# Optimization experiments

Measured on AMD Instinct MI355X. Metric: run time of the kernel, lower is better.

Reference implementation:

```python
import jax, jax.numpy as jnp
import numpy as np
import math

B, S, D, H = 2, 2048, 768, 12
DK = D // H


def setup_inputs() -> dict:
    key = jax.random.key(0)
    ks = jax.random.split(key, 8)
    scale = 1.0 / math.sqrt(D)  # xavier-ish scale for weights
    inp = {
        "query": jax.random.normal(ks[0], (B, S, D), jnp.float32),
        "key": jax.random.normal(ks[1], (B, S, D), jnp.float32),
        "value": jax.random.normal(ks[2], (B, S, D), jnp.float32),
        # causal mask: True = masked (matches torch masked_fill_ semantics)
        "mask": jnp.broadcast_to(jnp.triu(jnp.ones((S, S), bool), k=1), (B, S, S)),
        "wq": jax.random.normal(ks[3], (D, D), jnp.float32) * scale,
        "wk": jax.random.normal(ks[4], (D, D), jnp.float32) * scale,
        "wv": jax.random.normal(ks[5], (D, D), jnp.float32) * scale,
        "wo": jax.random.normal(ks[6], (D, D), jnp.float32) * scale,
        "bo": jnp.zeros((D,), jnp.float32),
    }
    return inp


def reference(query, key, value, mask, wq, wk, wv, wo, bo):
    # nn.Linear stores weight [out, in]; y = x @ W^T
    def split_heads(x):  # [B,S,D] -> [B,H,S,DK]
        return x.reshape(B, S, H, DK).transpose(0, 2, 1, 3)

    q = split_heads(jnp.einsum('bsd,ed->bse', query, wq))
    k = split_heads(jnp.einsum('bsd,ed->bse', key, wk))
    v = split_heads(jnp.einsum('bsd,ed->bse', value, wv))

    scores = jnp.einsum('bhqd,bhkd->bhqk', q, k) / math.sqrt(DK)
    scores = jnp.where(mask[:, None, :, :], -jnp.inf, scores)
    attn = jax.nn.softmax(scores, axis=-1)  # dropout is identity in eval / p=0

    attended = jnp.einsum('bhqk,bhkd->bhqd', attn, v)
    attended = attended.transpose(0, 2, 1, 3).reshape(B, S, D)
    return jnp.einsum('bsd,ed->bse', attended, wo) + bo
```

## Files before the change

kernel.cpp:

```cpp
#include <hip/hip_runtime.h>

namespace {
constexpr int Sc = 2048, Dc = 768, Hc = 12, Mc = 4096;

using fragb = __attribute__((ext_vector_type(8))) short;
using f32x4 = __attribute__((ext_vector_type(4))) float;

#define MFMA16(A, B, C) __builtin_amdgcn_mfma_f32_16x16x32_bf16(A, B, C, 0, 0, 0)

__device__ __forceinline__ unsigned short bf16hi(float f) {
  unsigned int u = __float_as_uint(f);
  return (unsigned short)((u + 0x7fffu + ((u >> 16) & 1u)) >> 16);
}
__device__ __forceinline__ float fbf(unsigned short h) {
  return __uint_as_float((unsigned int)h << 16);
}
__device__ __forceinline__ unsigned int packsplit(float f) {
  unsigned short h = bf16hi(f);
  unsigned short l = bf16hi(f - fbf(h));
  return ((unsigned int)h << 16) | (unsigned int)l;
}
__device__ __forceinline__ void split8(const float* x, fragb& hv, fragb& lv) {
  union { fragb v; short s[8]; } h, l;
#pragma unroll
  for (int i = 0; i < 8; ++i) {
    unsigned short hh = bf16hi(x[i]);
    h.s[i] = (short)hh;
    l.s[i] = (short)bf16hi(x[i] - fbf(hh));
  }
  hv = h.v; lv = l.v;
}
__device__ __forceinline__ void unpack8(const unsigned int* u, fragb& hv, fragb& lv) {
  union { fragb v; short s[8]; } h, l;
#pragma unroll
  for (int i = 0; i < 8; ++i) {
    h.s[i] = (short)(u[i] >> 16);
    l.s[i] = (short)(u[i] & 0xffffu);
  }
  hv = h.v; lv = l.v;
}

template <int AMODE, int OMODE>
__global__ __launch_bounds__(256, 3) void proj_kernel(
    const void* __restrict__ Asrc, const float* __restrict__ W,
    const float* __restrict__ bias, void* __restrict__ Out)
{
  const int tid = threadIdx.x;
  const int lane = tid & 63, w = tid >> 6;
  const int g = lane >> 4, l15 = lane & 15;
  const int m0 = blockIdx.x * 64, n0 = blockIdx.y * 64;

  __shared__ __align__(16) short Ah[64][40], Al[64][40];
  __shared__ __align__(16) short Bh[64][40], Bl[64][40];

  f32x4 acc[4] = {};

  const int srow = tid >> 2;
  const int scol = (tid & 3) * 8;

  for (int k0 = 0; k0 < Dc; k0 += 32) {
    fragb ah_s, al_s, bh_s, bl_s;
    if (AMODE == 0) {
      const float* ap = (const float*)Asrc + (size_t)(m0 + srow) * Dc + k0 + scol;
      float4 v0 = *(const float4*)(ap);
      float4 v1 = *(const float4*)(ap + 4);
      float xa[8] = {v0.x, v0.y, v0.z, v0.w, v1.x, v1.y, v1.z, v1.w};
      split8(xa, ah_s, al_s);
    } else {
      const unsigned int* ap = (const unsigned int*)Asrc + (size_t)(m0 + srow) * Dc + k0 + scol;
      uint4 v0 = *(const uint4*)(ap);
      uint4 v1 = *(const uint4*)(ap + 4);
      unsigned int ua[8] = {v0.x, v0.y, v0.z, v0.w, v1.x, v1.y, v1.z, v1.w};
      unpack8(ua, ah_s, al_s);
    }
    {
      const float* wp = W + (size_t)(n0 + srow) * Dc + k0 + scol;
      float4 v0 = *(const float4*)(wp);
      float4 v1 = *(const float4*)(wp + 4);
      float xw[8] = {v0.x, v0.y, v0.z, v0.w, v1.x, v1.y, v1.z, v1.w};
      split8(xw, bh_s, bl_s);
    }
    __syncthreads();
    *(fragb*)&Ah[srow][scol] = ah_s;
    *(fragb*)&Al[srow][scol] = al_s;
    *(fragb*)&Bh[srow][scol] = bh_s;
    *(fragb*)&Bl[srow][scol] = bl_s;
    __syncthreads();

    const fragb aH = *(const fragb*)&Ah[16 * w + l15][8 * g];
    const fragb aL = *(const fragb*)&Al[16 * w + l15][8 * g];
#pragma unroll
    for (int nb = 0; nb < 4; ++nb) {
      const fragb bH = *(const fragb*)&Bh[nb * 16 + l15][8 * g];
      const fragb bL = *(const fragb*)&Bl[nb * 16 + l15][8 * g];
      acc[nb] = MFMA16(aH, bH, acc[nb]);
      acc[nb] = MFMA16(aH, bL, acc[nb]);
      acc[nb] = MFMA16(aL, bH, acc[nb]);
    }
  }

  const int mrow = m0 + 16 * w + 4 * g;
  if (OMODE == 2) {
#pragma unroll
    for (int nb = 0; nb < 4; ++nb) {
      const int n = n0 + nb * 16 + l15;
      const float bv = bias[n];
#pragma unroll
      for (int r = 0; r < 4; ++r)
        ((float*)Out)[(size_t)(mrow + r) * Dc + n] = acc[nb][r] + bv;
    }
  } else {
#pragma unroll
    for (int nb = 0; nb < 4; ++nb) {
      const int n = n0 + nb * 16 + l15;
      const int hh = n >> 6, dk = n & 63;
#pragma unroll
      for (int r = 0; r < 4; ++r) {
        const int m = mrow + r;
        const int bb = m >> 11, s = m & (Sc - 1);
        const size_t idx = (OMODE == 0)
            ? (((size_t)bb * Hc + hh) * Sc + s) * 64 + dk
            : (((size_t)bb * Hc + hh) * 64 + dk) * Sc + s;
        ((unsigned int*)Out)[idx] = packsplit(acc[nb][r]);
      }
    }
  }
}

__global__ __launch_bounds__(256, 3) void attn_kernel(
    const unsigned int* __restrict__ Qp, const unsigned int* __restrict__ Kp,
    const unsigned int* __restrict__ Vtg, unsigned int* __restrict__ att2)
{
  const int tid = threadIdx.x;
  const int lane = tid & 63, w = tid >> 6;
  const int g = lane >> 4, l15 = lane & 15;
  const int t = blockIdx.x;
  const int bh = blockIdx.y;
  const int b = bh / Hc, h = bh % Hc;

  const int qtile = (w < 2) ? t : (63 - t);
  const int qbase = qtile * 32 + (w & 1) * 16;
  const int ktmax = (qbase + 15) >> 6;
  const int NKT = ((Sc - 1 - 32 * t) >> 6) + 1;

  __shared__ __align__(16) short Ks_h[64][72], Ks_l[64][72];
  __shared__ __align__(16) short Vt_h[64][72], Vt_l[64][72];
  __shared__ __align__(16) short Ps[64][72];

  fragb qh[2], ql[2];
  {
    const unsigned int* qrow = Qp + ((size_t)bh * Sc + qbase + l15) * 64;
#pragma unroll
    for (int c = 0; c < 2; ++c) {
      uint4 v0 = *(const uint4*)(qrow + c * 32 + g * 8);
      uint4 v1 = *(const uint4*)(qrow + c * 32 + g * 8 + 4);
      unsigned int u[8] = {v0.x, v0.y, v0.z, v0.w, v1.x, v1.y, v1.z, v1.w};
      unpack8(u, qh[c], ql[c]);
    }
  }

  f32x4 oacc[4] = {};
  float m_run[4] = {-1e30f, -1e30f, -1e30f, -1e30f};
  float l_run[4] = {0.f, 0.f, 0.f, 0.f};

  const int srow = tid >> 2;
  const int scol = (tid & 3) * 16;

  for (int kt = 0; kt < NKT; ++kt) {
    const int k0 = kt * 64;
    uint4 ka[4], va[4];
    {
      const unsigned int* kp = Kp + ((size_t)bh * Sc + k0 + srow) * 64 + scol;
      const unsigned int* vp = Vtg + ((size_t)bh * 64 + srow) * Sc + k0 + scol;
#pragma unroll
      for (int u = 0; u < 4; ++u) {
        ka[u] = *(const uint4*)(kp + 4 * u);
        va[u] = *(const uint4*)(vp + 4 * u);
      }
    }
    __syncthreads();
    {
      fragb h0, l0, h1, l1;
      unsigned int u[8];
      u[0]=ka[0].x; u[1]=ka[0].y; u[2]=ka[0].z; u[3]=ka[0].w;
      u[4]=ka[1].x; u[5]=ka[1].y; u[6]=ka[1].z; u[7]=ka[1].w;
      unpack8(u, h0, l0);
      u[0]=ka[2].x; u[1]=ka[2].y; u[2]=ka[2].z; u[3]=ka[2].w;
      u[4]=ka[3].x; u[5]=ka[3].y; u[6]=ka[3].z; u[7]=ka[3].w;
      unpack8(u, h1, l1);
      *(fragb*)&Ks_h[srow][scol]     = h0;
      *(fragb*)&Ks_h[srow][scol + 8] = h1;
      *(fragb*)&Ks_l[srow][scol]     = l0;
      *(fragb*)&Ks_l[srow][scol + 8] = l1;
      u[0]=va[0].x; u[1]=va[0].y; u[2]=va[0].z; u[3]=va[0].w;
      u[4]=va[1].x; u[5]=va[1].y; u[6]=va[1].z; u[7]=va[1].w;
      unpack8(u, h0, l0);
      u[0]=va[2].x; u[1]=va[2].y; u[2]=va[2].z; u[3]=va[2].w;
      u[4]=va[3].x; u[5]=va[3].y; u[6]=va[3].z; u[7]=va[3].w;
      unpack8(u, h1, l1);
      *(fragb*)&Vt_h[srow][scol]     = h0;
      *(fragb*)&Vt_h[srow][scol + 8] = h1;
      *(fragb*)&Vt_l[srow][scol]     = l0;
      *(fragb*)&Vt_l[srow][scol + 8] = l1;
    }
    __syncthreads();

    if (kt <= ktmax) {
      f32x4 sacc[4] = {};
#pragma unroll
      for (int c = 0; c < 2; ++c) {
#pragma unroll
        for (int kb = 0; kb < 4; ++kb) {
          const fragb kH = *(const fragb*)&Ks_h[kb * 16 + l15][c * 32 + g * 8];
          const fragb kL = *(const fragb*)&Ks_l[kb * 16 + l15][c * 32 + g * 8];
          sacc[kb] = MFMA16(qh[c], kH, sacc[kb]);
          sacc[kb] = MFMA16(qh[c], kL, sacc[kb]);
          sacc[kb] = MFMA16(ql[c], kH, sacc[kb]);
        }
      }
      float p[4][4], mx[4];
#pragma unroll
      for (int r = 0; r < 4; ++r) {
        const int qrow = qbase + 4 * g + r;
#pragma unroll
        for (int kb = 0; kb < 4; ++kb) {
          const int kc = k0 + kb * 16 + l15;
          const float x = sacc[kb][r] * 0.125f;
          p[kb][r] = (kc > qrow) ? -1e30f : x;
        }
        mx[r] = fmaxf(fmaxf(p[0][r], p[1][r]), fmaxf(p[2][r], p[3][r]));
      }
#pragma unroll
      for (int off = 8; off > 0; off >>= 1)
#pragma unroll
        for (int r = 0; r < 4; ++r)
          mx[r] = fmaxf(mx[r], __shfl_xor(mx[r], off));
#pragma unroll
      for (int r = 0; r < 4; ++r) {
        const float mnew = fmaxf(m_run[r], mx[r]);
        const float alpha = __expf(m_run[r] - mnew);
        m_run[r] = mnew;
        float rs = 0.f;
#pragma unroll
        for (int kb = 0; kb < 4; ++kb) { p[kb][r] = __expf(p[kb][r] - mnew); rs += p[kb][r]; }
#pragma unroll
        for (int off = 8; off > 0; off >>= 1) rs += __shfl_xor(rs, off);
        l_run[r] = l_run[r] * alpha + rs;
#pragma unroll
        for (int db = 0; db < 4; ++db) oacc[db][r] *= alpha;
      }
      const int strip = 16 * w;
#pragma unroll
      for (int kb = 0; kb < 4; ++kb)
#pragma unroll
        for (int r = 0; r < 4; ++r)
          Ps[strip + 4 * g + r][kb * 16 + l15] = (short)bf16hi(p[kb][r]);
#pragma unroll
      for (int c = 0; c < 2; ++c) {
        const fragb pf = *(const fragb*)&Ps[strip + l15][c * 32 + g * 8];
#pragma unroll
        for (int db = 0; db < 4; ++db) {
          const fragb vH = *(const fragb*)&Vt_h[db * 16 + l15][c * 32 + g * 8];
          const fragb vL = *(const fragb*)&Vt_l[db * 16 + l15][c * 32 + g * 8];
          oacc[db] = MFMA16(pf, vH, oacc[db]);
          oacc[db] = MFMA16(pf, vL, oacc[db]);
        }
      }
    }
  }

#pragma unroll
  for (int r = 0; r < 4; ++r) {
    const float rl = 1.0f / l_run[r];
    const int s = qbase + 4 * g + r;
    unsigned int* orow = att2 + ((size_t)b * Sc + s) * Dc + h * 64 + l15;
#pragma unroll
    for (int db = 0; db < 4; ++db)
      orow[db * 16] = packsplit(oacc[db][r] * rl);
  }
}

}

extern "C" void kernel_launch(void* const* d_in, const int* in_sizes, int n_in,
                              void* d_out, int out_size, void* d_ws, size_t ws_size,
                              hipStream_t stream) {
  const float* q  = (const float*)d_in[0];
  const float* k  = (const float*)d_in[1];
  const float* v  = (const float*)d_in[2];
  const float* wq = (const float*)d_in[4];
  const float* wk = (const float*)d_in[5];
  const float* wv = (const float*)d_in[6];
  const float* wo = (const float*)d_in[7];
  const float* bo = (const float*)d_in[8];

  unsigned int* ws   = (unsigned int*)d_ws;
  const size_t NQ = (size_t)Mc * Dc;
  unsigned int* Qp   = ws;
  unsigned int* Kp   = ws + NQ;
  unsigned int* Vtg  = ws + 2 * NQ;
  unsigned int* att2 = ws + 3 * NQ;

  const dim3 blk(256);
  const dim3 gproj(Mc / 64, Dc / 64);
  const dim3 gattn(32, 2 * Hc);

  proj_kernel<0, 0><<<gproj, blk, 0, stream>>>(q, wq, nullptr, Qp);
  proj_kernel<0, 0><<<gproj, blk, 0, stream>>>(k, wk, nullptr, Kp);
  proj_kernel<0, 1><<<gproj, blk, 0, stream>>>(v, wv, nullptr, Vtg);
  attn_kernel<<<gattn, blk, 0, stream>>>(Qp, Kp, Vtg, att2);
  proj_kernel<1, 2><<<gproj, blk, 0, stream>>>(att2, wo, bo, d_out);
}
```

Before: 336.0 us.

## Store hi/lo bf16 planes separately and enlarge projection tile to 128 rows

Intermediate Q/K/V/attention tensors are now stored as two separate bf16 planes (hi and lo) instead of packed 32-bit words. This lets the attention and output-projection kernels copy tiles straight into shared memory without unpacking. The split now truncates instead of rounding to nearest. Projection blocks grow to 128x64 with B fragments reused across two M sub-tiles, and launch bounds move to 4 waves per SIMD. The cost is more scattered 2-byte stores in the projection epilogue and a small change in numerics from the truncating split.

```diff
diff --git a/kernel.cpp b/kernel.cpp
--- a/kernel.cpp
+++ b/kernel.cpp
@@ -8,128 +8,132 @@
 
 #define MFMA16(A, B, C) __builtin_amdgcn_mfma_f32_16x16x32_bf16(A, B, C, 0, 0, 0)
 
-__device__ __forceinline__ unsigned short bf16hi(float f) {
+__device__ __forceinline__ unsigned short bf16rne(float f) {
   unsigned int u = __float_as_uint(f);
   return (unsigned short)((u + 0x7fffu + ((u >> 16) & 1u)) >> 16);
 }
-__device__ __forceinline__ float fbf(unsigned short h) {
-  return __uint_as_float((unsigned int)h << 16);
-}
-__device__ __forceinline__ unsigned int packsplit(float f) {
-  unsigned short h = bf16hi(f);
-  unsigned short l = bf16hi(f - fbf(h));
-  return ((unsigned int)h << 16) | (unsigned int)l;
-}
-__device__ __forceinline__ void split8(const float* x, fragb& hv, fragb& lv) {
-  union { fragb v; short s[8]; } h, l;
-#pragma unroll
-  for (int i = 0; i < 8; ++i) {
-    unsigned short hh = bf16hi(x[i]);
-    h.s[i] = (short)hh;
-    l.s[i] = (short)bf16hi(x[i] - fbf(hh));
-  }
-  hv = h.v; lv = l.v;
-}
-__device__ __forceinline__ void unpack8(const unsigned int* u, fragb& hv, fragb& lv) {
-  union { fragb v; short s[8]; } h, l;
-#pragma unroll
-  for (int i = 0; i < 8; ++i) {
-    h.s[i] = (short)(u[i] >> 16);
-    l.s[i] = (short)(u[i] & 0xffffu);
-  }
-  hv = h.v; lv = l.v;
+__device__ __forceinline__ void splitt(float f, unsigned short& h, unsigned short& l) {
+  const unsigned int u = __float_as_uint(f);
+  h = (unsigned short)(u >> 16);
+  const float r = f - __uint_as_float(u & 0xffff0000u);
+  l = (unsigned short)(__float_as_uint(r) >> 16);
 }
 
 template <int AMODE, int OMODE>
-__global__ __launch_bounds__(256, 3) void proj_kernel(
-    const void* __restrict__ Asrc, const float* __restrict__ W,
-    const float* __restrict__ bias, void* __restrict__ Out)
+__global__ __launch_bounds__(256, 4) void proj_kernel(
+    const void* __restrict__ Asrc_h, const void* __restrict__ Asrc_l,
+    const float* __restrict__ W, const float* __restrict__ bias,
+    unsigned short* __restrict__ Oh, unsigned short* __restrict__ Ol,
+    float* __restrict__ Ofp)
 {
   const int tid = threadIdx.x;
   const int lane = tid & 63, w = tid >> 6;
   const int g = lane >> 4, l15 = lane & 15;
-  const int m0 = blockIdx.x * 64, n0 = blockIdx.y * 64;
-
-  __shared__ __align__(16) short Ah[64][40], Al[64][40];
-  __shared__ __align__(16) short Bh[64][40], Bl[64][40];
-
-  f32x4 acc[4] = {};
-
-  const int srow = tid >> 2;
-  const int scol = (tid & 3) * 8;
+  const int m0 = blockIdx.x * 128, n0 = blockIdx.y * 64;
+
+  __shared__ __align__(16) unsigned short Ah[128][40], Al[128][40];
+  __shared__ __align__(16) unsigned short Bh[64][40],  Bl[64][40];
+
+  f32x4 acc[2][4] = {};
+
+  const int arow = tid >> 1;
+  const int acol = (tid & 1) * 16;
+  const int brow = tid >> 2;
+  const int bcol = (tid & 3) * 8;
 
   for (int k0 = 0; k0 < Dc; k0 += 32) {
-    fragb ah_s, al_s, bh_s, bl_s;
+    unsigned short ah[16], al[16], bh[8], bl[8];
     if (AMODE == 0) {
-      const float* ap = (const float*)Asrc + (size_t)(m0 + srow) * Dc + k0 + scol;
-      float4 v0 = *(const float4*)(ap);
-      float4 v1 = *(const float4*)(ap + 4);
-      float xa[8] = {v0.x, v0.y, v0.z, v0.w, v1.x, v1.y, v1.z, v1.w};
-      split8(xa, ah_s, al_s);
+      const float* ap = (const float*)Asrc_h + (size_t)(m0 + arow) * Dc + k0 + acol;
+#pragma unroll
+      for (int i = 0; i < 16; i += 4) {
+        const float4 v = *(const float4*)(ap + i);
+        splitt(v.x, ah[i+0], al[i+0]); splitt(v.y, ah[i+1], al[i+1]);
+        splitt(v.z, ah[i+2], al[i+2]); splitt(v.w, ah[i+3], al[i+3]);
+      }
     } else {
-      const unsigned int* ap = (const unsigned int*)Asrc + (size_t)(m0 + srow) * Dc + k0 + scol;
-      uint4 v0 = *(const uint4*)(ap);
-      uint4 v1 = *(const uint4*)(ap + 4);
-      unsigned int ua[8] = {v0.x, v0.y, v0.z, v0.w, v1.x, v1.y, v1.z, v1.w};
-      unpack8(ua, ah_s, al_s);
+      const unsigned short* aph = (const unsigned short*)Asrc_h + (size_t)(m0 + arow) * Dc + k0 + acol;
+      const unsigned short* apl = (const unsigned short*)Asrc_l + (size_t)(m0 + arow) * Dc + k0 + acol;
+      *(uint4*)&ah[0] = *(const uint4*)(aph);
+      *(uint4*)&ah[8] = *(const uint4*)(aph + 8);
+      *(uint4*)&al[0] = *(const uint4*)(apl);
+      *(uint4*)&al[8] = *(const uint4*)(apl + 8);
     }
     {
-      const float* wp = W + (size_t)(n0 + srow) * Dc + k0 + scol;
-      float4 v0 = *(const float4*)(wp);
-      float4 v1 = *(const float4*)(wp + 4);
-      float xw[8] = {v0.x, v0.y, v0.z, v0.w, v1.x, v1.y, v1.z, v1.w};
-      split8(xw, bh_s, bl_s);
+      const float* wp = W + (size_t)(n0 + brow) * Dc + k0 + bcol;
+#pragma unroll
+      for (int i = 0; i < 8; i += 4) {
+        const float4 v = *(const float4*)(wp + i);
+        splitt(v.x, bh[i+0], bl[i+0]); splitt(v.y, bh[i+1], bl[i+1]);
+        splitt(v.z, bh[i+2], bl[i+2]); splitt(v.w, bh[i+3], bl[i+3]);
+      }
     }
     __syncthreads();
-    *(fragb*)&Ah[srow][scol] = ah_s;
-    *(fragb*)&Al[srow][scol] = al_s;
-    *(fragb*)&Bh[srow][scol] = bh_s;
-    *(fragb*)&Bl[srow][scol] = bl_s;
+    *(uint4*)&Ah[arow][acol]     = *(uint4*)&ah[0];
+    *(uint4*)&Ah[arow][acol + 8] = *(uint4*)&ah[8];
+    *(uint4*)&Al[arow][acol]     = *(uint4*)&al[0];
+    *(uint4*)&Al[arow][acol + 8] = *(uint4*)&al[8];
+    *(uint4*)&Bh[brow][bcol]     = *(uint4*)&bh[0];
+    *(uint4*)&Bl[brow][bcol]     = *(uint4*)&bl[0];
     __syncthreads();
 
-    const fragb aH = *(const fragb*)&Ah[16 * w + l15][8 * g];
-    const fragb aL = *(const fragb*)&Al[16 * w + l15][8 * g];
+    fragb bHf[4], bLf[4];
 #pragma unroll
     for (int nb = 0; nb < 4; ++nb) {
-      const fragb bH = *(const fragb*)&Bh[nb * 16 + l15][8 * g];
-      const fragb bL = *(const fragb*)&Bl[nb * 16 + l15][8 * g];
-      acc[nb] = MFMA16(aH, bH, acc[nb]);
-      acc[nb] = MFMA16(aH, bL, acc[nb]);
-      acc[nb] = MFMA16(aL, bH, acc[nb]);
-    }
-  }
-
-  const int mrow = m0 + 16 * w + 4 * g;
-  if (OMODE == 2) {
-#pragma unroll
-    for (int nb = 0; nb < 4; ++nb) {
-      const int n = n0 + nb * 16 + l15;
-      const float bv = bias[n];
-#pragma unroll
-      for (int r = 0; r < 4; ++r)
-        ((float*)Out)[(size_t)(mrow + r) * Dc + n] = acc[nb][r] + bv;
-    }
-  } else {
-#pragma unroll
-    for (int nb = 0; nb < 4; ++nb) {
-      const int n = n0 + nb * 16 + l15;
-      const int hh = n >> 6, dk = n & 63;
-#pragma unroll
-      for (int r = 0; r < 4; ++r) {
-        const int m = mrow + r;
-        const int bb = m >> 11, s = m & (Sc - 1);
-        const size_t idx = (OMODE == 0)
-            ? (((size_t)bb * Hc + hh) * Sc + s) * 64 + dk
-            : (((size_t)bb * Hc + hh) * 64 + dk) * Sc + s;
-        ((unsigned int*)Out)[idx] = packsplit(acc[nb][r]);
+      bHf[nb] = *(const fragb*)&Bh[nb * 16 + l15][8 * g];
+      bLf[nb] = *(const fragb*)&Bl[nb * 16 + l15][8 * g];
+    }
+#pragma unroll
+    for (int s = 0; s < 2; ++s) {
+      const fragb aH = *(const fragb*)&Ah[32 * w + 16 * s + l15][8 * g];
+      const fragb aL = *(const fragb*)&Al[32 * w + 16 * s + l15][8 * g];
+#pragma unroll
+      for (int nb = 0; nb < 4; ++nb) {
+        acc[s][nb] = MFMA16(aH, bHf[nb], acc[s][nb]);
+        acc[s][nb] = MFMA16(aH, bLf[nb], acc[s][nb]);
+        acc[s][nb] = MFMA16(aL, bHf[nb], acc[s][nb]);
+      }
+    }
+  }
+
+#pragma unroll
+  for (int s = 0; s < 2; ++s) {
+    const int mrow = m0 + 32 * w + 16 * s + 4 * g;
+    if (OMODE == 2) {
+#pragma unroll
+      for (int nb = 0; nb < 4; ++nb) {
+        const int n = n0 + nb * 16 + l15;
+        const float bv = bias[n];
+#pragma unroll
+        for (int r = 0; r < 4; ++r)
+          Ofp[(size_t)(mrow + r) * Dc + n] = acc[s][nb][r] + bv;
+      }
+    } else {
+#pragma unroll
+      for (int nb = 0; nb < 4; ++nb) {
+        const int n = n0 + nb * 16 + l15;
+        const int hh = n >> 6, dk = n & 63;
+#pragma unroll
+        for (int r = 0; r < 4; ++r) {
+          const int m = mrow + r;
+          const int bb = m >> 11, ss = m & (Sc - 1);
+          const size_t idx = (OMODE == 0)
+              ? (((size_t)bb * Hc + hh) * Sc + ss) * 64 + dk
+              : (((size_t)bb * Hc + hh) * 64 + dk) * Sc + ss;
+          unsigned short h, l;
+          splitt(acc[s][nb][r], h, l);
+          Oh[idx] = h; Ol[idx] = l;
+        }
       }
     }
   }
 }
 
 __global__ __launch_bounds__(256, 3) void attn_kernel(
-    const unsigned int* __restrict__ Qp, const unsigned int* __restrict__ Kp,
-    const unsigned int* __restrict__ Vtg, unsigned int* __restrict__ att2)
+    const unsigned short* __restrict__ Qh, const unsigned short* __restrict__ Ql,
+    const unsigned short* __restrict__ Kh, const unsigned short* __restrict__ Kl,
+    const unsigned short* __restrict__ Vth, const unsigned short* __restrict__ Vtl,
+    unsigned short* __restrict__ Aoh, unsigned short* __restrict__ Aol)
 {
   const int tid = threadIdx.x;
   const int lane = tid & 63, w = tid >> 6;
@@ -143,19 +147,18 @@
   const int ktmax = (qbase + 15) >> 6;
   const int NKT = ((Sc - 1 - 32 * t) >> 6) + 1;
 
-  __shared__ __align__(16) short Ks_h[64][72], Ks_l[64][72];
-  __shared__ __align__(16) short Vt_h[64][72], Vt_l[64][72];
-  __shared__ __align__(16) short Ps[64][72];
-
-  fragb qh[2], ql[2];
+  __shared__ __align__(16) unsigned short Ks_h[64][72], Ks_l[64][72];
+  __shared__ __align__(16) unsigned short Vt_h[64][72], Vt_l[64][72];
+  __shared__ __align__(16) unsigned short Ps[64][72];
+
+  fragb qfh[2], qfl[2];
   {
-    const unsigned int* qrow = Qp + ((size_t)bh * Sc + qbase + l15) * 64;
+    const unsigned short* qrh = Qh + ((size_t)bh * Sc + qbase + l15) * 64;
+    const unsigned short* qrl = Ql + ((size_t)bh * Sc + qbase + l15) * 64;
 #pragma unroll
     for (int c = 0; c < 2; ++c) {
-      uint4 v0 = *(const uint4*)(qrow + c * 32 + g * 8);
-      uint4 v1 = *(const uint4*)(qrow + c * 32 + g * 8 + 4);
-      unsigned int u[8] = {v0.x, v0.y, v0.z, v0.w, v1.x, v1.y, v1.z, v1.w};
-      unpack8(u, qh[c], ql[c]);
+      qfh[c] = *(const fragb*)(qrh + c * 32 + g * 8);
+      qfl[c] = *(const fragb*)(qrl + c * 32 + g * 8);
     }
   }
 
@@ -168,41 +171,26 @@
 
   for (int kt = 0; kt < NKT; ++kt) {
     const int k0 = kt * 64;
-    uint4 ka[4], va[4];
+    uint4 st[8];
     {
-      const unsigned int* kp = Kp + ((size_t)bh * Sc + k0 + srow) * 64 + scol;
-      const unsigned int* vp = Vtg + ((size_t)bh * 64 + srow) * Sc + k0 + scol;
-#pragma unroll
-      for (int u = 0; u < 4; ++u) {
-        ka[u] = *(const uint4*)(kp + 4 * u);
-        va[u] = *(const uint4*)(vp + 4 * u);
-      }
+      const unsigned short* kph = Kh  + ((size_t)bh * Sc + k0 + srow) * 64 + scol;
+      const unsigned short* kpl = Kl  + ((size_t)bh * Sc + k0 + srow) * 64 + scol;
+      const unsigned short* vph = Vth + ((size_t)bh * 64 + srow) * Sc + k0 + scol;
+      const unsigned short* vpl = Vtl + ((size_t)bh * 64 + srow) * Sc + k0 + scol;
+      st[0] = *(const uint4*)(kph);  st[1] = *(const uint4*)(kph + 8);
+      st[2] = *(const uint4*)(kpl);  st[3] = *(const uint4*)(kpl + 8);
+      st[4] = *(const uint4*)(vph);  st[5] = *(const uint4*)(vph + 8);
+      st[6] = *(const uint4*)(vpl);  st[7] = *(const uint4*)(vpl + 8);
     }
     __syncthreads();
-    {
-      fragb h0, l0, h1, l1;
-      unsigned int u[8];
-      u[0]=ka[0].x; u[1]=ka[0].y; u[2]=ka[0].z; u[3]=ka[0].w;
-      u[4]=ka[1].x; u[5]=ka[1].y; u[6]=ka[1].z; u[7]=ka[1].w;
-      unpack8(u, h0, l0);
-      u[0]=ka[2].x; u[1]=ka[2].y; u[2]=ka[2].z; u[3]=ka[2].w;
-      u[4]=ka[3].x; u[5]=ka[3].y; u[6]=ka[3].z; u[7]=ka[3].w;
-      unpack8(u, h1, l1);
-      *(fragb*)&Ks_h[srow][scol]     = h0;
-      *(fragb*)&Ks_h[srow][scol + 8] = h1;
-      *(fragb*)&Ks_l[srow][scol]     = l0;
-      *(fragb*)&Ks_l[srow][scol + 8] = l1;
-      u[0]=va[0].x; u[1]=va[0].y; u[2]=va[0].z; u[3]=va[0].w;
-      u[4]=va[1].x; u[5]=va[1].y; u[6]=va[1].z; u[7]=va[1].w;
-      unpack8(u, h0, l0);
-      u[0]=va[2].x; u[1]=va[2].y; u[2]=va[2].z; u[3]=va[2].w;
-      u[4]=va[3].x; u[5]=va[3].y; u[6]=va[3].z; u[7]=va[3].w;
-      unpack8(u, h1, l1);
-      *(fragb*)&Vt_h[srow][scol]     = h0;
-      *(fragb*)&Vt_h[srow][scol + 8] = h1;
-      *(fragb*)&Vt_l[srow][scol]     = l0;
-      *(fragb*)&Vt_l[srow][scol + 8] = l1;
-    }
+    *(uint4*)&Ks_h[srow][scol]     = st[0];
+    *(uint4*)&Ks_h[srow][scol + 8] = st[1];
+    *(uint4*)&Ks_l[srow][scol]     = st[2];
+    *(uint4*)&Ks_l[srow][scol + 8] = st[3];
+    *(uint4*)&Vt_h[srow][scol]     = st[4];
+    *(uint4*)&Vt_h[srow][scol + 8] = st[5];
+    *(uint4*)&Vt_l[srow][scol]     = st[6];
+    *(uint4*)&Vt_l[srow][scol + 8] = st[7];
     __syncthreads();
 
     if (kt <= ktmax) {
@@ -213,9 +201,9 @@
         for (int kb = 0; kb < 4; ++kb) {
           const fragb kH = *(const fragb*)&Ks_h[kb * 16 + l15][c * 32 + g * 8];
           const fragb kL = *(const fragb*)&Ks_l[kb * 16 + l15][c * 32 + g * 8];
-          sacc[kb] = MFMA16(qh[c], kH, sacc[kb]);
-          sacc[kb] = MFMA16(qh[c], kL, sacc[kb]);
-          sacc[kb] = MFMA16(ql[c], kH, sacc[kb]);
+          sacc[kb] = MFMA16(qfh[c], kH, sacc[kb]);
+          sacc[kb] = MFMA16(qfh[c], kL, sacc[kb]);
+          sacc[kb] = MFMA16(qfl[c], kH, sacc[kb]);
         }
       }
       float p[4][4], mx[4];
@@ -254,7 +242,7 @@
       for (int kb = 0; kb < 4; ++kb)
 #pragma unroll
         for (int r = 0; r < 4; ++r)
-          Ps[strip + 4 * g + r][kb * 16 + l15] = (short)bf16hi(p[kb][r]);
+          Ps[strip + 4 * g + r][kb * 16 + l15] = bf16rne(p[kb][r]);
 #pragma unroll
       for (int c = 0; c < 2; ++c) {
         const fragb pf = *(const fragb*)&Ps[strip + l15][c * 32 + g * 8];
@@ -273,10 +261,14 @@
   for (int r = 0; r < 4; ++r) {
     const float rl = 1.0f / l_run[r];
     const int s = qbase + 4 * g + r;
-    unsigned int* orow = att2 + ((size_t)b * Sc + s) * Dc + h * 64 + l15;
-#pragma unroll
-    for (int db = 0; db < 4; ++db)
-      orow[db * 16] = packsplit(oacc[db][r] * rl);
+    const size_t base = ((size_t)b * Sc + s) * Dc + h * 64 + l15;
+#pragma unroll
+    for (int db = 0; db < 4; ++db) {
+      unsigned short hbits, lbits;
+      splitt(oacc[db][r] * rl, hbits, lbits);
+      Aoh[base + db * 16] = hbits;
+      Aol[base + db * 16] = lbits;
+    }
   }
 }
 
@@ -294,20 +286,24 @@
   const float* wo = (const float*)d_in[7];
   const float* bo = (const float*)d_in[8];
 
-  unsigned int* ws   = (unsigned int*)d_ws;
+  unsigned short* ws = (unsigned short*)d_ws;
   const size_t NQ = (size_t)Mc * Dc;
-  unsigned int* Qp   = ws;
-  unsigned int* Kp   = ws + NQ;
-  unsigned int* Vtg  = ws + 2 * NQ;
-  unsigned int* att2 = ws + 3 * NQ;
+  unsigned short* Qh_  = ws + 0 * NQ;
+  unsigned short* Ql_  = ws + 1 * NQ;
+  unsigned short* Kh_  = ws + 2 * NQ;
+  unsigned short* Kl_  = ws + 3 * NQ;
+  unsigned short* Vth_ = ws + 4 * NQ;
+  unsigned short* Vtl_ = ws + 5 * NQ;
+  unsigned short* Ath_ = ws + 6 * NQ;
+  unsigned short* Atl_ = ws + 7 * NQ;
 
   const dim3 blk(256);
-  const dim3 gproj(Mc / 64, Dc / 64);
+  const dim3 gproj(Mc / 128, Dc / 64);
   const dim3 gattn(32, 2 * Hc);
 
-  proj_kernel<0, 0><<<gproj, blk, 0, stream>>>(q, wq, nullptr, Qp);
-  proj_kernel<0, 0><<<gproj, blk, 0, stream>>>(k, wk, nullptr, Kp);
-  proj_kernel<0, 1><<<gproj, blk, 0, stream>>>(v, wv, nullptr, Vtg);
-  attn_kernel<<<gattn, blk, 0, stream>>>(Qp, Kp, Vtg, att2);
-  proj_kernel<1, 2><<<gproj, blk, 0, stream>>>(att2, wo, bo, d_out);
-}
+  proj_kernel<0, 0><<<gproj, blk, 0, stream>>>(q, nullptr, wq, nullptr, Qh_, Ql_, nullptr);
+  proj_kernel<0, 0><<<gproj, blk, 0, stream>>>(k, nullptr, wk, nullptr, Kh_, Kl_, nullptr);
+  proj_kernel<0, 1><<<gproj, blk, 0, stream>>>(v, nullptr, wv, nullptr, Vth_, Vtl_, nullptr);
+  attn_kernel<<<gattn, blk, 0, stream>>>(Qh_, Ql_, Kh_, Kl_, Vth_, Vtl_, Ath_, Atl_);
+  proj_kernel<1, 2><<<gproj, blk, 0, stream>>>(Ath_, Atl_, wo, bo, nullptr, nullptr, (float*)d_out);
+}
```

After: 506.5 us. +50.8%, slower.
